# Kernel optimization log

Hardware: AMD Instinct MI355X
Metric: run time of the kernel (lower is better)

The kernel has to match this reference:

```python
import jax, jax.numpy as jnp
import numpy as np

N_CLASSES = 101
STD = 0.05 * N_CLASSES  # std_smoothing * n_classes


def setup_inputs() -> dict:
    key = jax.random.key(0)
    k1, k2 = jax.random.split(key)
    B = 262144
    output = jax.random.normal(k1, (B, N_CLASSES), dtype=jnp.float32)
    target = jax.random.randint(k2, (B,), 0, N_CLASSES, dtype=jnp.int64)
    return {"output": output, "target": target}


def reference(output, target):
    # Gaussian pdf over classes centered at target, then row-normalized.
    # pdf constant factor cancels under normalization, so p = softmax(logits)
    # with logits = -(x - target)^2 / (2*std^2).
    x = jnp.arange(N_CLASSES, dtype=jnp.float32)  # [C]
    d = x[None, :] - target[:, None].astype(jnp.float32)  # [B, C]
    logits = -(d * d) / (2.0 * STD * STD)
    logp = jax.nn.log_softmax(logits, axis=-1)  # log model_prob
    p = jnp.exp(logp)  # model_prob
    # F.kl_div(input=output, target=p, reduction='sum') = sum(p * (log p - output))
    return jnp.sum(p * (logp - output.astype(jnp.float32)))
```

## Files before the change

kernel.cpp:

```cpp
#include <hip/hip_runtime.h>

#define N_CLASSES 101
#define TABLE_ELEMS (N_CLASSES * N_CLASSES)

__global__ void ls_init_tables(float* __restrict__ p_tab,
                               float* __restrict__ s1_tab,
                               float* __restrict__ result) {
    const int t = threadIdx.x;
    if (t == 0) result[0] = 0.0f;
    if (t < N_CLASSES) {
        const float std_v = 0.05f * (float)N_CLASSES;
        const float inv2s2 = 1.0f / (2.0f * std_v * std_v);
        float denom = 0.0f;
        for (int c = 0; c < N_CLASSES; ++c) {
            float d = (float)(c - t);
            denom += expf(-d * d * inv2s2);
        }
        const float L  = logf(denom);
        const float rd = 1.0f / denom;
        float s1 = 0.0f;
        for (int c = 0; c < N_CLASSES; ++c) {
            float d = (float)(c - t);
            float l = -d * d * inv2s2;
            float p = expf(l) * rd;
            p_tab[t * N_CLASSES + c] = p;
            s1 += p * (l - L);
        }
        s1_tab[t] = s1;
    }
}

__launch_bounds__(256)
__global__ void ls_kl_main(const float* __restrict__ out,
                           const int* __restrict__ target,
                           const float* __restrict__ p_tab,
                           const float* __restrict__ s1_tab,
                           float* __restrict__ result,
                           int total4) {
    __shared__ float p_lds[TABLE_ELEMS];
    __shared__ float s1_lds[N_CLASSES];
    __shared__ float wave_part[4];

    for (int i = threadIdx.x; i < TABLE_ELEMS; i += 256) p_lds[i] = p_tab[i];
    if (threadIdx.x < N_CLASSES) s1_lds[threadIdx.x] = s1_tab[threadIdx.x];
    __syncthreads();

    float acc = 0.0f;
    const int stride = gridDim.x * 256;
    for (int i4 = blockIdx.x * 256 + threadIdx.x; i4 < total4; i4 += stride) {
        const float4 v = reinterpret_cast<const float4*>(out)[i4];
        unsigned i0 = (unsigned)i4 * 4u;
        unsigned r = i0 / 101u;
        unsigned c = i0 - r * 101u;
        unsigned t = (unsigned)target[r];
        float vals[4] = {v.x, v.y, v.z, v.w};
#pragma unroll
        for (int j = 0; j < 4; ++j) {
            if (c == N_CLASSES) { c = 0u; ++r; t = (unsigned)target[r]; }
            if (c == 0u) acc += s1_lds[t];
            acc -= p_lds[t * N_CLASSES + c] * vals[j];
            ++c;
        }
    }

#pragma unroll
    for (int o = 32; o > 0; o >>= 1) acc += __shfl_down(acc, o, 64);
    const int wid  = threadIdx.x >> 6;
    const int lane = threadIdx.x & 63;
    if (lane == 0) wave_part[wid] = acc;
    __syncthreads();
    if (threadIdx.x == 0) {
        float s = wave_part[0] + wave_part[1] + wave_part[2] + wave_part[3];
        atomicAdd(result, s);
    }
}

extern "C" void kernel_launch(void* const* d_in, const int* in_sizes, int n_in,
                              void* d_out, int out_size, void* d_ws, size_t ws_size,
                              hipStream_t stream) {
    const float* output = (const float*)d_in[0];
    const int*   target = (const int*)d_in[1];
    float* result = (float*)d_out;

    float* p_tab  = (float*)d_ws;
    float* s1_tab = p_tab + TABLE_ELEMS;

    const int B = in_sizes[1];
    const long long total = (long long)B * N_CLASSES;
    const int total4 = (int)(total >> 2);

    ls_init_tables<<<1, 128, 0, stream>>>(p_tab, s1_tab, result);

    int grid = (total4 + 255) / 256;
    if (grid > 2048) grid = 2048;
    ls_kl_main<<<grid, 256, 0, stream>>>(output, target, p_tab, s1_tab, result, total4);
}
```

Measured before the change: 204.4 us.

## Compute Gaussian probabilities on the fly instead of an LDS table

Drops the 101x101 probability table staged in LDS and recomputes each probability with exp2f of the squared distance times a per-target reciprocal denominator. Each thread now handles 8 elements through two nontemporal float4 loads, and the sum is split across two accumulators. This removes the per-block LDS fill, its barrier and the large shared allocation, which should help occupancy. In exchange each element pays an integer divide, a target load and an exp instead of an LDS read.

```diff
diff --git a/kernel.cpp b/kernel.cpp
--- a/kernel.cpp
+++ b/kernel.cpp
@@ -1,11 +1,12 @@
 #include <hip/hip_runtime.h>
 
 #define N_CLASSES 101
-#define TABLE_ELEMS (N_CLASSES * N_CLASSES)
 
-__global__ void ls_init_tables(float* __restrict__ p_tab,
-                               float* __restrict__ s1_tab,
-                               float* __restrict__ result) {
+typedef float floatx4 __attribute__((ext_vector_type(4)));
+
+__global__ void ls_init(float* __restrict__ rd_tab,
+                        float* __restrict__ s1_tab,
+                        float* __restrict__ result) {
     const int t = threadIdx.x;
     if (t == 0) result[0] = 0.0f;
     if (t < N_CLASSES) {
@@ -22,10 +23,9 @@
         for (int c = 0; c < N_CLASSES; ++c) {
             float d = (float)(c - t);
             float l = -d * d * inv2s2;
-            float p = expf(l) * rd;
-            p_tab[t * N_CLASSES + c] = p;
-            s1 += p * (l - L);
+            s1 += expf(l) * rd * (l - L);
         }
+        rd_tab[t] = rd;
         s1_tab[t] = s1;
     }
 }
@@ -33,46 +33,42 @@
 __launch_bounds__(256)
 __global__ void ls_kl_main(const float* __restrict__ out,
                            const int* __restrict__ target,
-                           const float* __restrict__ p_tab,
+                           const float* __restrict__ rd_tab,
                            const float* __restrict__ s1_tab,
                            float* __restrict__ result,
-                           int total4) {
-    __shared__ float p_lds[TABLE_ELEMS];
-    __shared__ float s1_lds[N_CLASSES];
+                           unsigned total8) {
     __shared__ float wave_part[4];
+    const float NK2 = -(1.0f / (2.0f * 5.05f * 5.05f)) * 1.44269504088896340736f;
 
-    for (int i = threadIdx.x; i < TABLE_ELEMS; i += 256) p_lds[i] = p_tab[i];
-    if (threadIdx.x < N_CLASSES) s1_lds[threadIdx.x] = s1_tab[threadIdx.x];
-    __syncthreads();
-
-    float acc = 0.0f;
-    const int stride = gridDim.x * 256;
-    for (int i4 = blockIdx.x * 256 + threadIdx.x; i4 < total4; i4 += stride) {
-        const float4 v = reinterpret_cast<const float4*>(out)[i4];
-        unsigned i0 = (unsigned)i4 * 4u;
-        unsigned r = i0 / 101u;
-        unsigned c = i0 - r * 101u;
-        unsigned t = (unsigned)target[r];
-        float vals[4] = {v.x, v.y, v.z, v.w};
+    float acc0 = 0.0f, acc1 = 0.0f;
+    const unsigned stride = gridDim.x * blockDim.x;
+    for (unsigned g = blockIdx.x * blockDim.x + threadIdx.x; g < total8; g += stride) {
+        const floatx4* p4 = reinterpret_cast<const floatx4*>(out);
+        const floatx4 va = __builtin_nontemporal_load(p4 + 2u * g);
+        const floatx4 vb = __builtin_nontemporal_load(p4 + 2u * g + 1u);
+        const float v[8] = {va.x, va.y, va.z, va.w, vb.x, vb.y, vb.z, vb.w};
+        const unsigned i0 = g * 8u;
 #pragma unroll
-        for (int j = 0; j < 4; ++j) {
-            if (c == N_CLASSES) { c = 0u; ++r; t = (unsigned)target[r]; }
-            if (c == 0u) acc += s1_lds[t];
-            acc -= p_lds[t * N_CLASSES + c] * vals[j];
-            ++c;
+        for (int j = 0; j < 8; ++j) {
+            const unsigned i = i0 + (unsigned)j;
+            const unsigned r = i / 101u;
+            const unsigned c = i - r * 101u;
+            const int   t = target[r];
+            const int   d = (int)c - t;
+            const float p = exp2f((float)(d * d) * NK2) * rd_tab[t];
+            const float s = (c == 0u) ? s1_tab[t] : 0.0f;
+            if (j & 1) acc1 = acc1 + s - p * v[j];
+            else       acc0 = acc0 + s - p * v[j];
         }
     }
 
+    float acc = acc0 + acc1;
 #pragma unroll
     for (int o = 32; o > 0; o >>= 1) acc += __shfl_down(acc, o, 64);
-    const int wid  = threadIdx.x >> 6;
-    const int lane = threadIdx.x & 63;
-    if (lane == 0) wave_part[wid] = acc;
+    if ((threadIdx.x & 63) == 0) wave_part[threadIdx.x >> 6] = acc;
     __syncthreads();
-    if (threadIdx.x == 0) {
-        float s = wave_part[0] + wave_part[1] + wave_part[2] + wave_part[3];
-        atomicAdd(result, s);
-    }
+    if (threadIdx.x == 0)
+        atomicAdd(result, wave_part[0] + wave_part[1] + wave_part[2] + wave_part[3]);
 }
 
 extern "C" void kernel_launch(void* const* d_in, const int* in_sizes, int n_in,
@@ -82,16 +78,16 @@
     const int*   target = (const int*)d_in[1];
     float* result = (float*)d_out;
 
-    float* p_tab  = (float*)d_ws;
-    float* s1_tab = p_tab + TABLE_ELEMS;
+    float* rd_tab = (float*)d_ws;
+    float* s1_tab = rd_tab + N_CLASSES;
 
     const int B = in_sizes[1];
-    const long long total = (long long)B * N_CLASSES;
-    const int total4 = (int)(total >> 2);
+    const unsigned long long total = (unsigned long long)B * N_CLASSES;
+    const unsigned total8 = (unsigned)(total / 8u);
 
-    ls_init_tables<<<1, 128, 0, stream>>>(p_tab, s1_tab, result);
+    ls_init<<<1, 128, 0, stream>>>(rd_tab, s1_tab, result);
 
-    int grid = (total4 + 255) / 256;
-    if (grid > 2048) grid = 2048;
-    ls_kl_main<<<grid, 256, 0, stream>>>(output, target, p_tab, s1_tab, result, total4);
+    unsigned grid = (total8 + 255u) / 256u;
+    if (grid > 2048u) grid = 2048u;
+    ls_kl_main<<<grid, 256, 0, stream>>>(output, target, rd_tab, s1_tab, result, total8);
 }
```

Measured after the change: 191.5 us. 1.07x faster.
